# Kernel tuning notes

Measured on AMD Instinct MI355X. Metric: run time of the kernel, lower is better.

## Reference

```python
import jax, jax.numpy as jnp
import numpy as np


def setup_inputs() -> dict:
    key = jax.random.key(0)
    k1, k2, k3, k4 = jax.random.split(key, 4)
    B, D, U = 16, 2048, 37
    inputs = jax.random.normal(k1, (B, D), dtype=jnp.float32)
    matrix = jax.random.normal(k2, (D, D), dtype=jnp.float32) * 0.05
    weight = jax.random.normal(k3, (U, D, D), dtype=jnp.float32) * 0.05
    bias = jax.random.normal(k4, (U,), dtype=jnp.float32) * 0.05
    return {"inputs": inputs, "matrix": matrix, "weight": weight, "bias": bias}


def reference(inputs, matrix, weight, bias):
    # inputs: (B, D); matrix: (D, D); weight: (U, D, D); bias: (U,)
    B, D = inputs.shape
    idx = jnp.arange(D)
    # maps = ones((B, D, D)) with per-row diagonal replaced by inputs[b]
    maps = jnp.ones((B, D, D), dtype=inputs.dtype).at[:, idx, idx].set(inputs)
    # masked multiply by learned matrix (broadcast over batch) then relu
    masked = jax.nn.relu(matrix[None, :, :] * maps)  # (B, D, D)
    # outer-product-then-reduce collapses to a direct contraction per unit:
    # conv[b, u] = sum_ij masked[b, i, j] * weight[u, i, j]
    conv = jnp.einsum('bij,uij->bu', masked, weight)
    return conv + bias[None, :]
```

## Files before the change

### kernel.cpp

```cpp
#include <hip/hip_runtime.h>

constexpr int BB = 16;
constexpr int D  = 2048;
constexpr int U  = 37;
constexpr long long DD = (long long)D * D;

constexpr int TPB = 256;
constexpr int C   = 512;
constexpr int F4_PER_BLOCK  = (int)(DD / 4 / C);
constexpr int F4_PER_THREAD = F4_PER_BLOCK / TPB;

__global__ __launch_bounds__(TPB) void base_reduce_kernel(
    const float* __restrict__ matrix,
    const float* __restrict__ weight,
    float* __restrict__ partial)
{
    const int c = blockIdx.x;
    const long long base4 = (long long)c * F4_PER_BLOCK + threadIdx.x;
    const float4* __restrict__ m4 = (const float4*)matrix;

    float4 m[F4_PER_THREAD];
#pragma unroll
    for (int it = 0; it < F4_PER_THREAD; ++it) {
        float4 t = m4[base4 + (long long)it * TPB];
        m[it].x = fmaxf(t.x, 0.f);
        m[it].y = fmaxf(t.y, 0.f);
        m[it].z = fmaxf(t.z, 0.f);
        m[it].w = fmaxf(t.w, 0.f);
    }

    __shared__ float lpart[U];
    if (threadIdx.x < U) lpart[threadIdx.x] = 0.f;
    __syncthreads();

    for (int u = 0; u < U; ++u) {
        const float4* __restrict__ w4 = (const float4*)(weight + (long long)u * DD);
        float acc = 0.f;
#pragma unroll
        for (int it = 0; it < F4_PER_THREAD; ++it) {
            float4 w = w4[base4 + (long long)it * TPB];
            acc = fmaf(m[it].x, w.x, acc);
            acc = fmaf(m[it].y, w.y, acc);
            acc = fmaf(m[it].z, w.z, acc);
            acc = fmaf(m[it].w, w.w, acc);
        }
#pragma unroll
        for (int off = 32; off > 0; off >>= 1)
            acc += __shfl_down(acc, off, 64);
        if ((threadIdx.x & 63) == 0)
            atomicAdd(&lpart[u], acc);
    }

    __syncthreads();
    if (threadIdx.x < U)
        partial[(long long)threadIdx.x * C + c] = lpart[threadIdx.x];
}

__global__ __launch_bounds__(TPB) void diag_finish_kernel(
    const float* __restrict__ inputs,
    const float* __restrict__ matrix,
    const float* __restrict__ weight,
    const float* __restrict__ bias,
    const float* __restrict__ partial,
    float* __restrict__ out)
{
    const int u = blockIdx.x;
    const int b = blockIdx.y;

    float acc = 0.f;
    for (int i = threadIdx.x; i < D; i += TPB) {
        float mm = matrix[(long long)i * (D + 1)];
        float w  = weight[(long long)u * DD + (long long)i * (D + 1)];
        float x  = inputs[b * D + i];
        acc += (fmaxf(mm * x, 0.f) - fmaxf(mm, 0.f)) * w;
    }
    for (int c = threadIdx.x; c < C; c += TPB)
        acc += partial[(long long)u * C + c];

#pragma unroll
    for (int off = 32; off > 0; off >>= 1)
        acc += __shfl_down(acc, off, 64);

    __shared__ float smem[TPB / 64];
    if ((threadIdx.x & 63) == 0) smem[threadIdx.x >> 6] = acc;
    __syncthreads();
    if (threadIdx.x == 0) {
        float t = 0.f;
#pragma unroll
        for (int w = 0; w < TPB / 64; ++w) t += smem[w];
        out[b * U + u] = t + bias[u];
    }
}

extern "C" void kernel_launch(void* const* d_in, const int* in_sizes, int n_in,
                              void* d_out, int out_size, void* d_ws, size_t ws_size,
                              hipStream_t stream) {
    const float* inputs = (const float*)d_in[0];
    const float* matrix = (const float*)d_in[1];
    const float* weight = (const float*)d_in[2];
    const float* bias   = (const float*)d_in[3];
    float* out     = (float*)d_out;
    float* partial = (float*)d_ws;

    base_reduce_kernel<<<dim3(C), TPB, 0, stream>>>(matrix, weight, partial);
    diag_finish_kernel<<<dim3(U, BB), TPB, 0, stream>>>(inputs, matrix, weight, bias,
                                                        partial, out);
}
```

Before: 795.7 us.

## Fully unroll unit loop, extract weight diagonal in main kernel, double block count

The streaming kernel now uses 1024 blocks and fully unrolls the 37-unit loop, keeping 37 accumulators so all weight loads can be issued back to back. Shuffle reductions and the shared-memory atomics are deferred to the end. The main kernel also copies each unit's weight diagonal into a compact workspace array, so the finish kernel no longer makes strided diagonal reads across the 620MB weight tensor per (u,b) block. This risks register pressure under launch_bounds occupancy 4, and diagonal extraction is spread across blocks with a small divergent write.

```diff
diff --git a/kernel.cpp b/kernel.cpp
--- a/kernel.cpp
+++ b/kernel.cpp
@@ -6,14 +6,16 @@
 constexpr long long DD = (long long)D * D;
 
 constexpr int TPB = 256;
-constexpr int C   = 512;
+constexpr int C   = 1024;
 constexpr int F4_PER_BLOCK  = (int)(DD / 4 / C);
 constexpr int F4_PER_THREAD = F4_PER_BLOCK / TPB;
 
-__global__ __launch_bounds__(TPB) void base_reduce_kernel(
+
+__global__ __launch_bounds__(TPB, 4) void base_diag_kernel(
     const float* __restrict__ matrix,
     const float* __restrict__ weight,
-    float* __restrict__ partial)
+    float* __restrict__ partial,
+    float* __restrict__ wdiag)
 {
     const int c = blockIdx.x;
     const long long base4 = (long long)c * F4_PER_BLOCK + threadIdx.x;
@@ -29,39 +31,52 @@
         m[it].w = fmaxf(t.w, 0.f);
     }
 
+    float acc[U];
+#pragma unroll
+    for (int u = 0; u < U; ++u) acc[u] = 0.f;
+
+#pragma unroll
+    for (int u = 0; u < U; ++u) {
+        const float4* __restrict__ w4 = (const float4*)(weight + (long long)u * DD);
+        if (threadIdx.x < 2) {
+            const int i = 2 * c + (int)threadIdx.x;
+            wdiag[u * D + i] = weight[(long long)u * DD + (long long)i * (D + 1)];
+        }
+#pragma unroll
+        for (int it = 0; it < F4_PER_THREAD; ++it) {
+            float4 w = w4[base4 + (long long)it * TPB];
+            acc[u] = fmaf(m[it].x, w.x, acc[u]);
+            acc[u] = fmaf(m[it].y, w.y, acc[u]);
+            acc[u] = fmaf(m[it].z, w.z, acc[u]);
+            acc[u] = fmaf(m[it].w, w.w, acc[u]);
+        }
+    }
+
     __shared__ float lpart[U];
     if (threadIdx.x < U) lpart[threadIdx.x] = 0.f;
     __syncthreads();
-
+#pragma unroll
     for (int u = 0; u < U; ++u) {
-        const float4* __restrict__ w4 = (const float4*)(weight + (long long)u * DD);
-        float acc = 0.f;
-#pragma unroll
-        for (int it = 0; it < F4_PER_THREAD; ++it) {
-            float4 w = w4[base4 + (long long)it * TPB];
-            acc = fmaf(m[it].x, w.x, acc);
-            acc = fmaf(m[it].y, w.y, acc);
-            acc = fmaf(m[it].z, w.z, acc);
-            acc = fmaf(m[it].w, w.w, acc);
-        }
 #pragma unroll
         for (int off = 32; off > 0; off >>= 1)
-            acc += __shfl_down(acc, off, 64);
-        if ((threadIdx.x & 63) == 0)
-            atomicAdd(&lpart[u], acc);
+            acc[u] += __shfl_down(acc[u], off, 64);
     }
-
+    if ((threadIdx.x & 63) == 0) {
+#pragma unroll
+        for (int u = 0; u < U; ++u)
+            atomicAdd(&lpart[u], acc[u]);
+    }
     __syncthreads();
     if (threadIdx.x < U)
         partial[(long long)threadIdx.x * C + c] = lpart[threadIdx.x];
 }
 
-__global__ __launch_bounds__(TPB) void diag_finish_kernel(
+__global__ __launch_bounds__(TPB) void finish_kernel(
     const float* __restrict__ inputs,
     const float* __restrict__ matrix,
-    const float* __restrict__ weight,
     const float* __restrict__ bias,
     const float* __restrict__ partial,
+    const float* __restrict__ wdiag,
     float* __restrict__ out)
 {
     const int u = blockIdx.x;
@@ -70,12 +85,12 @@
     float acc = 0.f;
     for (int i = threadIdx.x; i < D; i += TPB) {
         float mm = matrix[(long long)i * (D + 1)];
-        float w  = weight[(long long)u * DD + (long long)i * (D + 1)];
+        float wd = wdiag[u * D + i];
         float x  = inputs[b * D + i];
-        acc += (fmaxf(mm * x, 0.f) - fmaxf(mm, 0.f)) * w;
+        acc += (fmaxf(mm * x, 0.f) - fmaxf(mm, 0.f)) * wd;
     }
-    for (int c = threadIdx.x; c < C; c += TPB)
-        acc += partial[(long long)u * C + c];
+    for (int cc = threadIdx.x; cc < C; cc += TPB)
+        acc += partial[(long long)u * C + cc];
 
 #pragma unroll
     for (int off = 32; off > 0; off >>= 1)
@@ -101,8 +116,9 @@
     const float* bias   = (const float*)d_in[3];
     float* out     = (float*)d_out;
     float* partial = (float*)d_ws;
+    float* wdiag   = (float*)d_ws + (long long)U * C;
 
-    base_reduce_kernel<<<dim3(C), TPB, 0, stream>>>(matrix, weight, partial);
-    diag_finish_kernel<<<dim3(U, BB), TPB, 0, stream>>>(inputs, matrix, weight, bias,
-                                                        partial, out);
+    base_diag_kernel<<<dim3(C), TPB, 0, stream>>>(matrix, weight, partial, wdiag);
+    finish_kernel<<<dim3(U, BB), TPB, 0, stream>>>(inputs, matrix, bias,
+                                                   partial, wdiag, out);
 }
```

Result: slower. 1.020 ms (+28.2%).
